# Kernel tuning notes

Hardware: AMD Instinct MI355X
Metric: run time of the kernel (lower is better)

The kernel has to match this reference:

```python
import jax, jax.numpy as jnp
import numpy as np

EPS = 1e-5

def _binact(x):
    # ReActNet piecewise-polynomial sign with straight-through estimator
    p = jnp.where(x < -1.0, -1.0,
        jnp.where(x < 0.0, x * x + 2.0 * x,
        jnp.where(x < 1.0, -x * x + 2.0 * x, 1.0)))
    return jax.lax.stop_gradient(jnp.sign(x) - p) + p

def _binweight(w):
    # per-output-channel scaling * sign(w), STE through clipped weights
    scale = jax.lax.stop_gradient(jnp.mean(jnp.abs(w), axis=(1, 2, 3), keepdims=True))
    bw = scale * jnp.sign(w)
    cl = jnp.clip(w, -1.0, 1.0)
    return jax.lax.stop_gradient(bw - cl) + cl

def _conv(x, w, stride, pad):
    return jax.lax.conv_general_dilated(x, w, (stride, stride), [(pad, pad), (pad, pad)],
                                        dimension_numbers=('NCHW', 'OIHW', 'NCHW'))

def _bn(x, gamma, beta, mean, var):
    inv = gamma / jnp.sqrt(var + EPS)
    return x * inv[None, :, None, None] + (beta - mean * inv)[None, :, None, None]

def _prelu(x, a):
    return jnp.where(x > 0, x, a[None, :, None, None] * x)

def _bias(x, b):
    return x + b[None, :, None, None]

def setup_inputs() -> dict:
    key = jax.random.key(0)
    ks = jax.random.split(key, 12)
    B, C, H, W = 32, 256, 28, 28
    d = {}
    d['x'] = jax.random.normal(ks[0], (B, C, H, W), jnp.float32)
    d['loss'] = jnp.zeros((), jnp.float32)
    # learnable biases (move11/12/13, move21/22/23)
    for i, name in enumerate(['b11', 'b12', 'b13', 'b21', 'b22', 'b23']):
        d[name] = 0.01 * jax.random.normal(ks[1 + i], (C,), jnp.float32)
    # binary conv weights: 3x3 (C->C, groups=1) and 1x1 (C->C)
    d['w1'] = 0.05 * jax.random.normal(ks[7], (C, C, 3, 3), jnp.float32)
    d['w2'] = 0.05 * jax.random.normal(ks[8], (C, C, 1, 1), jnp.float32)
    # batchnorm params (inference-style running stats)
    d['g1'] = jnp.ones((C,), jnp.float32); d['be1'] = jnp.zeros((C,), jnp.float32)
    d['m1'] = 0.1 * jax.random.normal(ks[9], (C,), jnp.float32)
    d['v1'] = 0.5 + jax.random.uniform(ks[10], (C,), jnp.float32)
    d['g2'] = jnp.ones((C,), jnp.float32); d['be2'] = jnp.zeros((C,), jnp.float32)
    d['m2'] = 0.1 * jax.random.normal(ks[11], (C,), jnp.float32)
    d['v2'] = 0.5 + jax.random.uniform(jax.random.fold_in(key, 99), (C,), jnp.float32)
    # PReLU slopes
    d['a1'] = 0.25 * jnp.ones((C,), jnp.float32)
    d['a2'] = 0.25 * jnp.ones((C,), jnp.float32)
    return d

def reference(x, loss, b11, b12, b13, b21, b22, b23, w1, w2,
              g1, be1, m1, v1, g2, be2, m2, v2, a1, a2):
    # branch 1: bias -> sign act -> 3x3 binary conv -> BN -> residual -> bias/PReLU/bias
    out1 = _binact(_bias(x, b11))
    out1 = _conv(out1, _binweight(w1), 1, 1)
    out1 = _bn(out1, g1, be1, m1, v1)
    out1 = out1 + x  # adaptive_add: shapes match (stride=1, inp==oup)
    out1 = _bias(_prelu(_bias(out1, b12), a1), b13)
    # branch 2: bias -> sign act -> 1x1 binary conv -> BN -> residual -> bias/PReLU/bias
    out2 = _binact(_bias(out1, b21))
    out2 = _conv(out2, _binweight(w2), 1, 0)
    out2 = _bn(out2, g2, be2, m2, v2)
    out2 = out2 + out1
    out2 = _bias(_prelu(_bias(out2, b22), a2), b23)
    return (out2, loss)
```

## Files before the change

kernel.cpp:

```cpp
#include <hip/hip_runtime.h>
#include <hip/hip_bf16.h>


typedef unsigned short u16;
typedef unsigned char  u8;
typedef unsigned int   u32;
typedef unsigned long long u64;
typedef float f32x4 __attribute__((ext_vector_type(4)));
typedef long  long2v __attribute__((ext_vector_type(2)));
typedef int   v8i  __attribute__((ext_vector_type(8)));
typedef float v16f __attribute__((ext_vector_type(16)));

__device__ __forceinline__ float b2f(u16 u) {
  union { unsigned int i; float f; } c; c.i = ((unsigned int)u) << 16; return c.f;
}
__device__ __forceinline__ u16 f2b(float f) {
  unsigned int u = __builtin_bit_cast(unsigned int, f);
  unsigned int r = (u + 0x7FFFu + ((u >> 16) & 1u)) >> 16;
  return (u16)r;
}
__device__ __forceinline__ u8 f2sign8(float v) {
  return (v > 0.f) ? 0x38 : ((v < 0.f) ? 0xB8 : 0x00);
}
__device__ __forceinline__ v8i mkv8(long2v a, long2v b) {
  union { long2v l[2]; v8i v; } u; u.l[0] = a; u.l[1] = b; return u.v;
}

__global__ __launch_bounds__(256) void prep_kernel(
    const float* __restrict__ w1, const float* __restrict__ w2,
    const float* __restrict__ g1, const float* __restrict__ be1,
    const float* __restrict__ m1, const float* __restrict__ v1,
    const float* __restrict__ g2, const float* __restrict__ be2,
    const float* __restrict__ m2, const float* __restrict__ v2,
    u8* __restrict__ w1T, u8* __restrict__ w2T,
    float* __restrict__ ab,
    float* __restrict__ lossdst, const float* __restrict__ lossin)
{
  __shared__ float wrow[2304];
  __shared__ float red[256];
  const int t = threadIdx.x;
  const int blk = blockIdx.x;
  float s = 0.f;
  if (blk < 256) {
    const int o = blk;
    const float4* src = (const float4*)(w1 + o * 2304);
#pragma unroll
    for (int i = 0; i < 3; ++i) {
      int c = i * 256 + t;
      if (c < 576) {
        float4 v = src[c];
        wrow[c * 4 + 0] = v.x; wrow[c * 4 + 1] = v.y;
        wrow[c * 4 + 2] = v.z; wrow[c * 4 + 3] = v.w;
        s += fabsf(v.x) + fabsf(v.y) + fabsf(v.z) + fabsf(v.w);
      }
    }
  } else {
    const int o = blk - 256;
    float v = w2[o * 256 + t];
    wrow[t] = v;
    s = fabsf(v);
  }
  red[t] = s;
  __syncthreads();
  for (int st = 128; st > 0; st >>= 1) { if (t < st) red[t] += red[t + st]; __syncthreads(); }
  if (blk < 256) {
    const int o = blk;
    for (int it = t; it < 288; it += 256) {
      int tap = it >> 5, ci8 = it & 31;
      u64 pack = 0;
#pragma unroll
      for (int k = 0; k < 8; ++k)
        pack |= ((u64)f2sign8(wrow[(ci8 * 8 + k) * 9 + tap])) << (8 * k);
      int c64 = ci8 >> 3, kh = (ci8 >> 2) & 1, slot = ci8 & 3;
      *(u64*)(w1T + (size_t)((tap * 4 + c64) * 2 + kh) * 8192 + o * 32 + slot * 8) = pack;
    }
    if (t == 0) {
      float scale = red[0] / 2304.f;
      float inv = g1[o] / sqrtf(v1[o] + 1e-5f);
      ab[o]       = scale * inv;
      ab[256 + o] = be1[o] - m1[o] * inv;
    }
  } else {
    const int o = blk - 256;
    if (t < 32) {
      u64 pack = 0;
#pragma unroll
      for (int k = 0; k < 8; ++k)
        pack |= ((u64)f2sign8(wrow[t * 8 + k])) << (8 * k);
      int c64 = t >> 3, kh = (t >> 2) & 1, slot = t & 3;
      *(u64*)(w2T + (size_t)(c64 * 2 + kh) * 8192 + o * 32 + slot * 8) = pack;
    }
    if (t == 0) {
      float scale = red[0] / 256.f;
      float inv = g2[o] / sqrtf(v2[o] + 1e-5f);
      ab[512 + o] = scale * inv;
      ab[768 + o] = be2[o] - m2[o] * inv;
    }
  }
  if (blk == 0 && t == 0) lossdst[0] = lossin[0];
}

__global__ __launch_bounds__(512, 1) void fused_kernel(
    const float* __restrict__ x, const float* __restrict__ b11,
    const u8* __restrict__ w1T, const u8* __restrict__ w2T,
    const float* __restrict__ ab,
    const float* __restrict__ b12, const float* __restrict__ a1,
    const float* __restrict__ b13, const float* __restrict__ b21,
    const float* __restrict__ b22, const float* __restrict__ a2,
    const float* __restrict__ b23,
    float* __restrict__ dout)
{
  __shared__ __align__(16) u8 win[51200];
  __shared__ float bsh[256];

  const int t = threadIdx.x;
  const int w = t >> 6;
  const int l = t & 63;
  const int l31 = l & 31;
  const int h32 = l >> 5;
  const int mg = w & 1;
  const int ng = w >> 1;
  const int pxblk = blockIdx.x;
  const int img = pxblk / 7;
  const int rowgrp = pxblk % 7;

  float al1[2], bt1[2], pA1[2], pS1[2], pB1[2], p21[2];
  float al2[2], bt2[2], pA2[2], pS2[2], pB2[2];
  int Ov[2];
#pragma unroll
  for (int nf = 0; nf < 2; ++nf) {
    int O = ng * 64 + nf * 32 + l31;
    Ov[nf] = O;
    al1[nf] = ab[O];       bt1[nf] = ab[256 + O];
    al2[nf] = ab[512 + O]; bt2[nf] = ab[768 + O];
    pA1[nf] = b12[O]; pS1[nf] = a1[O]; pB1[nf] = b13[O]; p21[nf] = b21[O];
    pA2[nf] = b22[O]; pS2[nf] = a2[O]; pB2[nf] = b23[O];
  }

  int basepix[2];
#pragma unroll
  for (int mi = 0; mi < 2; ++mi) {
    int pm = (mg * 2 + mi) * 32 + l31;
    int r = (pm * 293) >> 13;
    basepix[mi] = r * 30 + (pm - 28 * r);
  }

  char* wl = (char*)win;

  v16f acc[2][2];
  v16f zero16 = {0.f,0.f,0.f,0.f,0.f,0.f,0.f,0.f,0.f,0.f,0.f,0.f,0.f,0.f,0.f,0.f};
  f32x4 zero4 = {0.f, 0.f, 0.f, 0.f};
#pragma unroll
  for (int mi = 0; mi < 2; ++mi)
#pragma unroll
    for (int nf = 0; nf < 2; ++nf) acc[mi][nf] = zero16;

  if (t < 256) bsh[t] = b11[t];
#pragma unroll
  for (int i = 0; i < 7; ++i) {
    int c = i * 512 + t;
    if (c < 3200) *(f32x4*)(wl + c * 16) = zero4;
  }
  __syncthreads();

#pragma unroll 1
  for (int wr = 0; wr < 6; ++wr) {
    int r_img = rowgrp * 4 - 1 + wr;
    if ((unsigned)r_img < 28u) {
#pragma unroll
      for (int it = 0; it < 4; ++it) {
        int u = it * 512 + t;
        if (u < 1792) {
          int ci = u / 7;
          int p4 = u - ci * 7;
          float4 v = *(const float4*)(x + ((size_t)(img * 256 + ci)) * 784 + r_img * 28 + p4 * 4);
          float bb = bsh[ci];
          float vv[4] = {v.x, v.y, v.z, v.w};
          int pbase = wr * 30 + 1 + p4 * 4;
#pragma unroll
          for (int k = 0; k < 4; ++k) {
            int wp = pbase + k;
            wl[wp * 256 + (ci ^ ((wp & 15) << 4))] = f2sign8(vv[k] + bb);
          }
        }
      }
    }
  }
  __syncthreads();

  auto LOADB3 = [&](long2v (*dst)[2], int s) {
    int sc = (s < 36) ? s : 0;
    const char* base = (const char*)w1T + (size_t)sc * 16384 + h32 * 8192;
#pragma unroll
    for (int nf = 0; nf < 2; ++nf) {
      const char* p = base + (ng * 64 + nf * 32 + l31) * 32;
      dst[nf][0] = *(const long2v*)(p);
      dst[nf][1] = *(const long2v*)(p + 16);
    }
  };
  auto DSA3 = [&](long2v (*dst)[2], int s) {
    int sc = (s < 36) ? s : 0;
    int tap = sc >> 2;
    int c64 = sc & 3;
    int ti = (tap * 11) >> 5;
    int tapoff = ti * 30 + (tap - 3 * ti);
    int off = c64 * 64 + h32 * 32;
#pragma unroll
    for (int mi = 0; mi < 2; ++mi) {
      int wp = basepix[mi] + tapoff;
      int sw = (wp & 15) << 4;
      const char* p = wl + wp * 256;
      dst[mi][0] = *(const long2v*)(p + ((off)      ^ sw));
      dst[mi][1] = *(const long2v*)(p + ((off + 16) ^ sw));
    }
  };
  auto COMP = [&](long2v (*a)[2], long2v (*bv)[2]) {
    __builtin_amdgcn_s_setprio(1);
#pragma unroll
    for (int mi = 0; mi < 2; ++mi) {
      v8i a8 = mkv8(a[mi][0], a[mi][1]);
#pragma unroll
      for (int nf = 0; nf < 2; ++nf)
        acc[mi][nf] = __builtin_amdgcn_mfma_scale_f32_32x32x64_f8f6f4(
            a8, mkv8(bv[nf][0], bv[nf][1]), acc[mi][nf],
            0, 0, 0, 0x7F7F7F7Fu, 0, 0x7F7F7F7Fu);
    }
    __builtin_amdgcn_s_setprio(0);
  };

  long2v A0[2][2], A1[2][2];
  long2v b0[2][2], b1[2][2], b2[2][2];
  DSA3(A0, 0); LOADB3(b0, 0); LOADB3(b1, 1);
#pragma unroll 1
  for (int i = 0; i < 6; ++i) {
    int p = i * 6;
    LOADB3(b2, p + 2); DSA3(A1, p + 1); COMP(A0, b0);
    LOADB3(b0, p + 3); DSA3(A0, p + 2); COMP(A1, b1);
    LOADB3(b1, p + 4); DSA3(A1, p + 3); COMP(A0, b2);
    LOADB3(b2, p + 5); DSA3(A0, p + 4); COMP(A1, b0);
    LOADB3(b0, p + 6); DSA3(A1, p + 5); COMP(A0, b1);
    LOADB3(b1, p + 7); DSA3(A0, p + 6); COMP(A1, b2);
  }
  __syncthreads();

  u32 pk[2][2][4][2];
#pragma unroll
  for (int mi = 0; mi < 2; ++mi) {
    int m = mg * 2 + mi;
#pragma unroll
    for (int rp = 0; rp < 4; ++rp) {
      int pixbase = m * 32 + 8 * rp + 4 * h32;
      bool valid = (m < 3) || (rp < 2);
#pragma unroll
      for (int nf = 0; nf < 2; ++nf) {
        int O = Ov[nf];
        float xv[4] = {0.f, 0.f, 0.f, 0.f};
        if (valid) {
          int hwm = rowgrp * 112 + pixbase;
          float4 xr = *(const float4*)(x + ((size_t)(img * 256 + O) * 784 + hwm));
          xv[0] = xr.x; xv[1] = xr.y; xv[2] = xr.z; xv[3] = xr.w;
        }
        float o1v[4];
#pragma unroll
        for (int reg = 0; reg < 4; ++reg) {
          int pix = pixbase + reg;
          float v = acc[mi][nf][rp * 4 + reg] * al1[nf] + bt1[nf] + xv[reg];
          float t1 = v + pA1[nf];
          t1 = (t1 > 0.f) ? t1 : pS1[nf] * t1;
          o1v[reg] = t1 + pB1[nf];
          wl[pix * 256 + (O ^ ((pix & 15) << 4))] = f2sign8(o1v[reg] + p21[nf]);
        }
        pk[mi][nf][rp][0] = (u32)f2b(o1v[0]) | ((u32)f2b(o1v[1]) << 16);
        pk[mi][nf][rp][1] = (u32)f2b(o1v[2]) | ((u32)f2b(o1v[3]) << 16);
      }
    }
  }
#pragma unroll
  for (int mi = 0; mi < 2; ++mi)
#pragma unroll
    for (int nf = 0; nf < 2; ++nf) acc[mi][nf] = zero16;

  asm volatile("s_waitcnt lgkmcnt(0)" ::: "memory");
  __builtin_amdgcn_s_barrier();

  auto LOADB1 = [&](long2v (*dst)[2], int sp) {
    const char* base = (const char*)w2T + (size_t)sp * 16384 + h32 * 8192;
#pragma unroll
    for (int nf = 0; nf < 2; ++nf) {
      const char* p = base + (ng * 64 + nf * 32 + l31) * 32;
      dst[nf][0] = *(const long2v*)(p);
      dst[nf][1] = *(const long2v*)(p + 16);
    }
  };
  auto DSA1 = [&](long2v (*dst)[2], int sp) {
    int off = sp * 64 + h32 * 32;
#pragma unroll
    for (int mi = 0; mi < 2; ++mi) {
      int pm = (mg * 2 + mi) * 32 + l31;
      int sw = (pm & 15) << 4;
      const char* p = wl + pm * 256;
      dst[mi][0] = *(const long2v*)(p + ((off)      ^ sw));
      dst[mi][1] = *(const long2v*)(p + ((off + 16) ^ sw));
    }
  };
  DSA1(A0, 0); LOADB1(b0, 0);
  DSA1(A1, 1); LOADB1(b1, 1); COMP(A0, b0);
  DSA1(A0, 2); LOADB1(b0, 2); COMP(A1, b1);
  DSA1(A1, 3); LOADB1(b1, 3); COMP(A0, b0);
  COMP(A1, b1);

#pragma unroll
  for (int mi = 0; mi < 2; ++mi) {
    int m = mg * 2 + mi;
#pragma unroll
    for (int rp = 0; rp < 4; ++rp) {
      bool valid = (m < 3) || (rp < 2);
      if (!valid) continue;
      int pixbase = m * 32 + 8 * rp + 4 * h32;
      int hwm = rowgrp * 112 + pixbase;
#pragma unroll
      for (int nf = 0; nf < 2; ++nf) {
        int O = Ov[nf];
        float res[4];
        res[0] = b2f((u16)(pk[mi][nf][rp][0] & 0xFFFF));
        res[1] = b2f((u16)(pk[mi][nf][rp][0] >> 16));
        res[2] = b2f((u16)(pk[mi][nf][rp][1] & 0xFFFF));
        res[3] = b2f((u16)(pk[mi][nf][rp][1] >> 16));
        float r4v[4];
#pragma unroll
        for (int reg = 0; reg < 4; ++reg) {
          float v = acc[mi][nf][rp * 4 + reg] * al2[nf] + bt2[nf] + res[reg];
          float t1 = v + pA2[nf];
          t1 = (t1 > 0.f) ? t1 : pS2[nf] * t1;
          r4v[reg] = t1 + pB2[nf];
        }
        float4 r4 = {r4v[0], r4v[1], r4v[2], r4v[3]};
        *(float4*)(dout + ((size_t)(img * 256 + O)) * 784 + hwm) = r4;
      }
    }
  }
}

extern "C" void kernel_launch(void* const* d_in, const int* in_sizes, int n_in,
                              void* d_out, int out_size, void* d_ws, size_t ws_size,
                              hipStream_t stream) {
  const float* x    = (const float*)d_in[0];
  const float* loss = (const float*)d_in[1];
  const float* b11  = (const float*)d_in[2];
  const float* b12  = (const float*)d_in[3];
  const float* b13  = (const float*)d_in[4];
  const float* b21  = (const float*)d_in[5];
  const float* b22  = (const float*)d_in[6];
  const float* b23  = (const float*)d_in[7];
  const float* w1   = (const float*)d_in[8];
  const float* w2   = (const float*)d_in[9];
  const float* g1   = (const float*)d_in[10];
  const float* be1  = (const float*)d_in[11];
  const float* m1   = (const float*)d_in[12];
  const float* v1   = (const float*)d_in[13];
  const float* g2   = (const float*)d_in[14];
  const float* be2  = (const float*)d_in[15];
  const float* m2   = (const float*)d_in[16];
  const float* v2   = (const float*)d_in[17];
  const float* a1   = (const float*)d_in[18];
  const float* a2   = (const float*)d_in[19];

  char* ws = (char*)d_ws;
  u8*    w1T = (u8*)(ws + 0ull);
  u8*    w2T = (u8*)(ws + 589824ull);
  float* ab  = (float*)(ws + 655360ull);

  float* out = (float*)d_out;

  prep_kernel<<<512, 256, 0, stream>>>(w1, w2, g1, be1, m1, v1, g2, be2, m2, v2,
                                       w1T, w2T, ab, out + (out_size - 1), loss);
  fused_kernel<<<224, 512, 0, stream>>>(x, b11, w1T, w2T, ab,
                                        b12, a1, b13, b21, b22, a2, b23, out);
}
```

Baseline: 43.64 us.

## Switch binary MFMA operands from FP8 to packed FP4 signs

Encodes binarized activations and weights as 4-bit FP4 values (±1, 0) instead of FP8 bytes, and uses the f8f6f4 scaled MFMA in FP4 mode. This halves the LDS activation window, the global weight footprint and per-step operand loads. The epilogue now packs channel pairs through a lane shuffle before writing sign nibbles to LDS, and the swizzle is redone for the 128-byte row stride. The extra shuffle and packing logic add instructions, and correctness depends on the nibble and channel ordering matching the FP4 operand layout.

```diff
diff --git a/kernel.cpp b/kernel.cpp
--- a/kernel.cpp
+++ b/kernel.cpp
@@ -19,8 +19,8 @@
   unsigned int r = (u + 0x7FFFu + ((u >> 16) & 1u)) >> 16;
   return (u16)r;
 }
-__device__ __forceinline__ u8 f2sign8(float v) {
-  return (v > 0.f) ? 0x38 : ((v < 0.f) ? 0xB8 : 0x00);
+__device__ __forceinline__ u32 f2sign4(float v) {
+  return (v > 0.f) ? 0x2u : ((v < 0.f) ? 0xAu : 0x0u);
 }
 __device__ __forceinline__ v8i mkv8(long2v a, long2v b) {
   union { long2v l[2]; v8i v; } u; u.l[0] = a; u.l[1] = b; return u.v;
@@ -67,12 +67,12 @@
     const int o = blk;
     for (int it = t; it < 288; it += 256) {
       int tap = it >> 5, ci8 = it & 31;
-      u64 pack = 0;
+      u32 pack = 0;
 #pragma unroll
       for (int k = 0; k < 8; ++k)
-        pack |= ((u64)f2sign8(wrow[(ci8 * 8 + k) * 9 + tap])) << (8 * k);
+        pack |= f2sign4(wrow[(ci8 * 8 + k) * 9 + tap]) << (4 * k);
       int c64 = ci8 >> 3, kh = (ci8 >> 2) & 1, slot = ci8 & 3;
-      *(u64*)(w1T + (size_t)((tap * 4 + c64) * 2 + kh) * 8192 + o * 32 + slot * 8) = pack;
+      *(u32*)(w1T + (size_t)((tap * 4 + c64) * 2 + kh) * 4096 + o * 16 + slot * 4) = pack;
     }
     if (t == 0) {
       float scale = red[0] / 2304.f;
@@ -83,12 +83,12 @@
   } else {
     const int o = blk - 256;
     if (t < 32) {
-      u64 pack = 0;
+      u32 pack = 0;
 #pragma unroll
       for (int k = 0; k < 8; ++k)
-        pack |= ((u64)f2sign8(wrow[t * 8 + k])) << (8 * k);
+        pack |= f2sign4(wrow[t * 8 + k]) << (4 * k);
       int c64 = t >> 3, kh = (t >> 2) & 1, slot = t & 3;
-      *(u64*)(w2T + (size_t)(c64 * 2 + kh) * 8192 + o * 32 + slot * 8) = pack;
+      *(u32*)(w2T + (size_t)(c64 * 2 + kh) * 4096 + o * 16 + slot * 4) = pack;
     }
     if (t == 0) {
       float scale = red[0] / 256.f;
@@ -110,7 +110,7 @@
     const float* __restrict__ b23,
     float* __restrict__ dout)
 {
-  __shared__ __align__(16) u8 win[51200];
+  __shared__ __align__(16) u8 win[26112];
   __shared__ float bsh[256];
 
   const int t = threadIdx.x;
@@ -150,6 +150,7 @@
   v16f acc[2][2];
   v16f zero16 = {0.f,0.f,0.f,0.f,0.f,0.f,0.f,0.f,0.f,0.f,0.f,0.f,0.f,0.f,0.f,0.f};
   f32x4 zero4 = {0.f, 0.f, 0.f, 0.f};
+  long2v zl2 = {0, 0};
 #pragma unroll
   for (int mi = 0; mi < 2; ++mi)
 #pragma unroll
@@ -157,9 +158,9 @@
 
   if (t < 256) bsh[t] = b11[t];
 #pragma unroll
-  for (int i = 0; i < 7; ++i) {
+  for (int i = 0; i < 4; ++i) {
     int c = i * 512 + t;
-    if (c < 3200) *(f32x4*)(wl + c * 16) = zero4;
+    if (c < 1632) *(f32x4*)(wl + c * 16) = zero4;
   }
   __syncthreads();
 
@@ -168,19 +169,23 @@
     int r_img = rowgrp * 4 - 1 + wr;
     if ((unsigned)r_img < 28u) {
 #pragma unroll
-      for (int it = 0; it < 4; ++it) {
+      for (int it = 0; it < 2; ++it) {
         int u = it * 512 + t;
-        if (u < 1792) {
-          int ci = u / 7;
-          int p4 = u - ci * 7;
-          float4 v = *(const float4*)(x + ((size_t)(img * 256 + ci)) * 784 + r_img * 28 + p4 * 4);
-          float bb = bsh[ci];
-          float vv[4] = {v.x, v.y, v.z, v.w};
+        if (u < 896) {
+          int c2 = (u * 9363) >> 16;
+          int p4 = u - c2 * 7;
+          const float* xb = x + ((size_t)(img * 256 + 2 * c2)) * 784 + r_img * 28 + p4 * 4;
+          float4 v0 = *(const float4*)(xb);
+          float4 v1 = *(const float4*)(xb + 784);
+          float b0v = bsh[2 * c2], b1v = bsh[2 * c2 + 1];
+          float lo[4] = {v0.x, v0.y, v0.z, v0.w};
+          float hi[4] = {v1.x, v1.y, v1.z, v1.w};
           int pbase = wr * 30 + 1 + p4 * 4;
 #pragma unroll
           for (int k = 0; k < 4; ++k) {
             int wp = pbase + k;
-            wl[wp * 256 + (ci ^ ((wp & 15) << 4))] = f2sign8(vv[k] + bb);
+            u8 byte = (u8)(f2sign4(lo[k] + b0v) | (f2sign4(hi[k] + b1v) << 4));
+            wl[wp * 128 + ((((c2 >> 4) ^ (wp & 7)) << 4) | (c2 & 15))] = byte;
           }
         }
       }
@@ -188,48 +193,43 @@
   }
   __syncthreads();
 
-  auto LOADB3 = [&](long2v (*dst)[2], int s) {
+  auto LOADB3 = [&](long2v* dst, int s) {
     int sc = (s < 36) ? s : 0;
-    const char* base = (const char*)w1T + (size_t)sc * 16384 + h32 * 8192;
-#pragma unroll
-    for (int nf = 0; nf < 2; ++nf) {
-      const char* p = base + (ng * 64 + nf * 32 + l31) * 32;
-      dst[nf][0] = *(const long2v*)(p);
-      dst[nf][1] = *(const long2v*)(p + 16);
-    }
-  };
-  auto DSA3 = [&](long2v (*dst)[2], int s) {
+    const char* base = (const char*)w1T + (size_t)sc * 8192 + h32 * 4096;
+#pragma unroll
+    for (int nf = 0; nf < 2; ++nf)
+      dst[nf] = *(const long2v*)(base + (ng * 64 + nf * 32 + l31) * 16);
+  };
+  auto DSA3 = [&](long2v* dst, int s) {
     int sc = (s < 36) ? s : 0;
     int tap = sc >> 2;
     int c64 = sc & 3;
     int ti = (tap * 11) >> 5;
     int tapoff = ti * 30 + (tap - 3 * ti);
-    int off = c64 * 64 + h32 * 32;
+    int slot = c64 * 2 + h32;
 #pragma unroll
     for (int mi = 0; mi < 2; ++mi) {
       int wp = basepix[mi] + tapoff;
-      int sw = (wp & 15) << 4;
-      const char* p = wl + wp * 256;
-      dst[mi][0] = *(const long2v*)(p + ((off)      ^ sw));
-      dst[mi][1] = *(const long2v*)(p + ((off + 16) ^ sw));
-    }
-  };
-  auto COMP = [&](long2v (*a)[2], long2v (*bv)[2]) {
+      dst[mi] = *(const long2v*)(wl + wp * 128 + ((slot ^ (wp & 7)) << 4));
+    }
+  };
+  auto COMP = [&](long2v* a, long2v* bv) {
     __builtin_amdgcn_s_setprio(1);
 #pragma unroll
     for (int mi = 0; mi < 2; ++mi) {
-      v8i a8 = mkv8(a[mi][0], a[mi][1]);
+      v8i a8 = mkv8(a[mi], zl2);
 #pragma unroll
       for (int nf = 0; nf < 2; ++nf)
         acc[mi][nf] = __builtin_amdgcn_mfma_scale_f32_32x32x64_f8f6f4(
-            a8, mkv8(bv[nf][0], bv[nf][1]), acc[mi][nf],
-            0, 0, 0, 0x7F7F7F7Fu, 0, 0x7F7F7F7Fu);
+            a8, mkv8(bv[nf], zl2), acc[mi][nf],
+            4, 4,
+            0, 0x7F7F7F7Fu, 0, 0x7F7F7F7Fu);
     }
     __builtin_amdgcn_s_setprio(0);
   };
 
-  long2v A0[2][2], A1[2][2];
-  long2v b0[2][2], b1[2][2], b2[2][2];
+  long2v A0[2], A1[2];
+  long2v b0[2], b1[2], b2[2];
   DSA3(A0, 0); LOADB3(b0, 0); LOADB3(b1, 1);
 #pragma unroll 1
   for (int i = 0; i < 6; ++i) {
@@ -261,14 +261,25 @@
           xv[0] = xr.x; xv[1] = xr.y; xv[2] = xr.z; xv[3] = xr.w;
         }
         float o1v[4];
+        u32 mynibs = 0;
 #pragma unroll
         for (int reg = 0; reg < 4; ++reg) {
-          int pix = pixbase + reg;
           float v = acc[mi][nf][rp * 4 + reg] * al1[nf] + bt1[nf] + xv[reg];
           float t1 = v + pA1[nf];
           t1 = (t1 > 0.f) ? t1 : pS1[nf] * t1;
           o1v[reg] = t1 + pB1[nf];
-          wl[pix * 256 + (O ^ ((pix & 15) << 4))] = f2sign8(o1v[reg] + p21[nf]);
+          mynibs |= f2sign4(o1v[reg] + p21[nf]) << (4 * reg);
+        }
+        u32 partner = __shfl_xor((int)mynibs, 1);
+        if ((l31 & 1) == 0) {
+          int c2 = O >> 1;
+#pragma unroll
+          for (int reg = 0; reg < 4; ++reg) {
+            int pix = pixbase + reg;
+            u8 byte = (u8)(((mynibs >> (4 * reg)) & 0xF) |
+                           (((partner >> (4 * reg)) & 0xF) << 4));
+            wl[pix * 128 + ((((c2 >> 4) ^ (pix & 7)) << 4) | (c2 & 15))] = byte;
+          }
         }
         pk[mi][nf][rp][0] = (u32)f2b(o1v[0]) | ((u32)f2b(o1v[1]) << 16);
         pk[mi][nf][rp][1] = (u32)f2b(o1v[2]) | ((u32)f2b(o1v[3]) << 16);
@@ -283,24 +294,18 @@
   asm volatile("s_waitcnt lgkmcnt(0)" ::: "memory");
   __builtin_amdgcn_s_barrier();
 
-  auto LOADB1 = [&](long2v (*dst)[2], int sp) {
-    const char* base = (const char*)w2T + (size_t)sp * 16384 + h32 * 8192;
-#pragma unroll
-    for (int nf = 0; nf < 2; ++nf) {
-      const char* p = base + (ng * 64 + nf * 32 + l31) * 32;
-      dst[nf][0] = *(const long2v*)(p);
-      dst[nf][1] = *(const long2v*)(p + 16);
-    }
-  };
-  auto DSA1 = [&](long2v (*dst)[2], int sp) {
-    int off = sp * 64 + h32 * 32;
+  auto LOADB1 = [&](long2v* dst, int sp) {
+    const char* base = (const char*)w2T + (size_t)sp * 8192 + h32 * 4096;
+#pragma unroll
+    for (int nf = 0; nf < 2; ++nf)
+      dst[nf] = *(const long2v*)(base + (ng * 64 + nf * 32 + l31) * 16);
+  };
+  auto DSA1 = [&](long2v* dst, int sp) {
+    int slot = sp * 2 + h32;
 #pragma unroll
     for (int mi = 0; mi < 2; ++mi) {
       int pm = (mg * 2 + mi) * 32 + l31;
-      int sw = (pm & 15) << 4;
-      const char* p = wl + pm * 256;
-      dst[mi][0] = *(const long2v*)(p + ((off)      ^ sw));
-      dst[mi][1] = *(const long2v*)(p + ((off + 16) ^ sw));
+      dst[mi] = *(const long2v*)(wl + pm * 128 + ((slot ^ (pm & 7)) << 4));
     }
   };
   DSA1(A0, 0); LOADB1(b0, 0);
@@ -367,8 +372,8 @@
 
   char* ws = (char*)d_ws;
   u8*    w1T = (u8*)(ws + 0ull);
-  u8*    w2T = (u8*)(ws + 589824ull);
-  float* ab  = (float*)(ws + 655360ull);
+  u8*    w2T = (u8*)(ws + 294912ull);
+  float* ab  = (float*)(ws + 327680ull);
 
   float* out = (float*)d_out;
 
```

New measurement: 40.04 us. -8.3%, faster.
